# Optimization experiments

Measured on AMD Instinct MI355X. Metric: run time of the kernel, lower is better.

The kernel has to match this reference:

```python
import jax, jax.numpy as jnp
import numpy as np

N, E, D, H = 50000, 800000, 128, 128


def _uniform_param(key, shape, fan_in):
    bound = 1.0 / np.sqrt(fan_in)
    return jax.random.uniform(key, shape, jnp.float32, -bound, bound)


def setup_inputs() -> dict:
    key = jax.random.key(0)
    ks = jax.random.split(key, 12)
    x = jax.random.normal(ks[0], (N, D), jnp.float32)
    xedge = jax.random.randint(ks[1], (2, E), 0, N, jnp.int64)
    y = jax.random.randint(ks[2], (N,), 0, 2, jnp.int32).astype(bool)
    return {
        "x": x,
        "xedge": xedge,
        "y": y,
        "pretrain": 0,
        # SAGEConv layer 1 (in=D, out=H): lin_l (with bias) applied to mean aggr, lin_r (no bias) to self
        "W1l": _uniform_param(ks[3], (D, H), D),
        "b1l": _uniform_param(ks[4], (H,), D),
        "W1r": _uniform_param(ks[5], (D, H), D),
        # SAGEConv layer 2 (in=H, out=H)
        "W2l": _uniform_param(ks[6], (H, H), H),
        "b2l": _uniform_param(ks[7], (H,), H),
        "W2r": _uniform_param(ks[8], (H, H), H),
        # Decoder weight [H, H]
        "Wdec": _uniform_param(ks[9], (H, H), H),
    }


def sage_conv(h, src, dst, Wl, bl, Wr, num_nodes):
    # gather neighbor features along edges, mean-aggregate by destination
    msgs = h[src]                                            # [E, d]
    agg = jax.ops.segment_sum(msgs, dst, num_segments=num_nodes)
    cnt = jax.ops.segment_sum(jnp.ones((src.shape[0],), h.dtype), dst,
                              num_segments=num_nodes)
    mean = agg / jnp.maximum(cnt, 1.0)[:, None]              # [N, d]
    return mean @ Wl + bl + h @ Wr                           # [N, out]


def reference(x, xedge, y, pretrain, W1l, b1l, W1r, W2l, b2l, W2r, Wdec):
    src, dst = xedge[0], xedge[1]
    n = x.shape[0]
    # Encoder: SAGE = conv1 -> relu -> (dropout: eval identity) -> conv2
    h = jax.nn.relu(sage_conv(x, src, dst, W1l, b1l, W1r, n))
    emb = sage_conv(h, src, dst, W2l, b2l, W2r, n)           # [N, H]
    # Decoder
    dx = emb @ Wdec                                          # [N, H]
    # BCEWithLogits: pos nodes target 1, neg nodes target 0, mean within each group
    ym = y.astype(dx.dtype)                                  # [N]
    n_pos = jnp.sum(ym)
    n_neg = n - n_pos
    hdim = dx.shape[1]
    sp_pos = jax.nn.softplus(-dx)   # bce(logit, 1)
    sp_neg = jax.nn.softplus(dx)    # bce(logit, 0)
    l2 = jnp.sum(sp_pos * ym[:, None]) / (jnp.maximum(n_pos, 1.0) * hdim)
    l1 = jnp.sum(sp_neg * (1.0 - ym)[:, None]) / (jnp.maximum(n_neg, 1.0) * hdim)
    return (l1 + l2, emb)
```

## Files before the change

kernel.cpp:

```cpp
#include <hip/hip_runtime.h>
#include <hip/hip_bf16.h>

#define NDIM 128
#define MROWS 32
#define BTHREADS 512
#define SCAN_CHUNK 1024

typedef __attribute__((ext_vector_type(8))) short short8;
typedef __attribute__((ext_vector_type(4))) float f32x4;

__device__ __forceinline__ float bf2f(__hip_bfloat16 v) { return __bfloat162float(v); }

__device__ __forceinline__ float ldf(const void* p, long i, int f32) {
    return f32 ? ((const float*)p)[i] : bf2f(((const __hip_bfloat16*)p)[i]);
}
__device__ __forceinline__ void stf(void* p, long i, int f32, float v) {
    if (f32) ((float*)p)[i] = v;
    else     ((__hip_bfloat16*)p)[i] = __float2bfloat16(v);
}
__device__ __forceinline__ short f2bf(float v) {
    __hip_bfloat16 h = __float2bfloat16(v);
    short s;
    __builtin_memcpy(&s, &h, 2);
    return s;
}
__device__ __forceinline__ float bflo(unsigned u) { u <<= 16; float f; __builtin_memcpy(&f, &u, 4); return f; }
__device__ __forceinline__ float bfhi(unsigned u) { u &= 0xffff0000u; float f; __builtin_memcpy(&f, &u, 4); return f; }
__device__ __forceinline__ unsigned packbf(float a, float b) {
    unsigned la = (unsigned short)f2bf(a);
    unsigned hb = (unsigned short)f2bf(b);
    return (hb << 16) | la;
}
__device__ __forceinline__ int aswz(int m, int k) {
    return m * NDIM + ((((k >> 3) ^ (m & 7)) << 3) | (k & 7));
}
__device__ __forceinline__ int wswz(int m, int p) {
    return m * 64 + ((((p >> 2) ^ (m & 7)) << 2) | (p & 3));
}

__global__ void detect_kernel(const int* __restrict__ xedge32,
                              const unsigned int* __restrict__ yw,
                              const unsigned short* __restrict__ xh,
                              int* __restrict__ flags, int* __restrict__ cnt,
                              float* __restrict__ accum, int* __restrict__ npos, int N) {
    const int gid = blockIdx.x * 256 + threadIdx.x;
    for (int i = gid; i < N; i += gridDim.x * 256) cnt[i] = 0;
    if (gid == 0) { accum[0] = 0.f; accum[1] = 0.f; npos[0] = 0; }
    if (blockIdx.x == 0) {
        __shared__ int se, sy, scount;
        const int t = threadIdx.x;
        if (t == 0) { se = 1; sy = 0; scount = 0; }
        __syncthreads();
        for (int i = t; i < 512; i += 256)
            if (xedge32[2 * i + 1] != 0) se = 0;
        for (int i = t; i < 1024; i += 256)
            if (yw[i] > 1u) sy = 1;
        int c = 0;
        for (int i = t; i < 1024; i += 256) {
            int ex = (xh[2 * i] >> 7) & 0xFF;
            if (ex >= 100 && ex <= 150) c++;
        }
        atomicAdd(&scount, c);
        __syncthreads();
        if (t == 0) { flags[0] = se; flags[1] = sy; flags[2] = (scount < 900) ? 1 : 0; }
    }
}


__global__ void prep_kernel(const void* __restrict__ x,
                            const void* __restrict__ W1l, const void* __restrict__ b1l,
                            const void* __restrict__ W1r, const void* __restrict__ W2l,
                            const void* __restrict__ b2l, const void* __restrict__ W2r,
                            const void* __restrict__ Wd, const int* __restrict__ flags,
                            short* __restrict__ T1l, short* __restrict__ T1r,
                            short* __restrict__ T2l, short* __restrict__ T2r,
                            short* __restrict__ Td, float* __restrict__ b1c,
                            float* __restrict__ b2c, unsigned* __restrict__ xb,
                            const int* __restrict__ xedge, int E,
                            int* __restrict__ cnt, int N) {
    const int wf = flags[2];
    const long idx = (long)blockIdx.x * 256 + threadIdx.x;
    if (idx < E) {
        int d = flags[0] ? xedge[2 * (E + idx)] : xedge[E + idx];
        atomicAdd(&cnt[d], 1);
    }
    if (idx < NDIM * NDIM) {
        int k = (int)(idx >> 7), n = (int)(idx & 127);
        int o = n * NDIM + k;
        T1l[o] = f2bf(ldf(W1l, idx, wf));
        T1r[o] = f2bf(ldf(W1r, idx, wf));
        T2l[o] = f2bf(ldf(W2l, idx, wf));
        T2r[o] = f2bf(ldf(W2r, idx, wf));
        Td [o] = f2bf(ldf(Wd , idx, wf));
        if (idx < NDIM) { b1c[idx] = ldf(b1l, idx, wf); b2c[idx] = ldf(b2l, idx, wf); }
    }
    if (wf) {
        const long np = (long)N * 64;
        const long stride = (long)gridDim.x * 256;
        for (long p = idx; p < np; p += stride) {
            float2 v = ((const float2*)x)[p];
            xb[p] = packbf(v.x, v.y);
        }
    }
}


__global__ void scan_partial(const int* __restrict__ cnt, int* __restrict__ bsum, int N) {
    __shared__ int red[256];
    const int t = threadIdx.x;
    const long base = (long)blockIdx.x * SCAN_CHUNK + (long)t * 4;
    int s = 0;
#pragma unroll
    for (int i = 0; i < 4; ++i) { long idx = base + i; if (idx < N) s += cnt[idx]; }
    red[t] = s;
    __syncthreads();
    for (int off = 128; off >= 1; off >>= 1) {
        if (t < off) red[t] += red[t + off];
        __syncthreads();
    }
    if (t == 0) bsum[blockIdx.x] = red[0];
}

__global__ void scan_bsums(const int* __restrict__ bsum, int* __restrict__ boff,
                           int B, int* __restrict__ rowptr, int N) {
    __shared__ int part[1024];
    const int t = threadIdx.x;
    int v = (t < B) ? bsum[t] : 0;
    part[t] = v;
    __syncthreads();
    for (int off = 1; off < 1024; off <<= 1) {
        int u = (t >= off) ? part[t - off] : 0;
        __syncthreads();
        part[t] += u;
        __syncthreads();
    }
    if (t < B) boff[t] = part[t] - v;
    if (t == 1023) rowptr[N] = part[1023];
}

__global__ void scan_scatter(int* __restrict__ cnt, const int* __restrict__ boff,
                             int* __restrict__ rowptr, int N) {
    __shared__ int tsum[256];
    const int t = threadIdx.x;
    const long base = (long)blockIdx.x * SCAN_CHUNK + (long)t * 4;
    int loc[4];
    int s = 0;
#pragma unroll
    for (int i = 0; i < 4; ++i) {
        long idx = base + i;
        int c = (idx < N) ? cnt[idx] : 0;
        loc[i] = s;
        s += c;
    }
    tsum[t] = s;
    __syncthreads();
    for (int off = 1; off < 256; off <<= 1) {
        int u = (t >= off) ? tsum[t - off] : 0;
        __syncthreads();
        tsum[t] += u;
        __syncthreads();
    }
    const int texcl = tsum[t] - s;
    const int b0 = boff[blockIdx.x];
#pragma unroll
    for (int i = 0; i < 4; ++i) {
        long idx = base + i;
        if (idx < N) {
            int v = b0 + texcl + loc[i];
            rowptr[idx] = v;
            cnt[idx] = v;
        }
    }
}

__global__ void fill_kernel(const int* __restrict__ xedge, int E,
                            const int* __restrict__ flags,
                            int* __restrict__ cur, int* __restrict__ col) {
    int e = blockIdx.x * blockDim.x + threadIdx.x;
    if (e >= E) return;
    const int e64 = flags[0];
    int s = e64 ? xedge[2 * e] : xedge[e];
    int d = e64 ? xedge[2 * (E + e)] : xedge[E + e];
    int p = atomicAdd(&cur[d], 1);
    col[p] = s;
}


template <bool RELU, int OUTMODE>
__global__ __launch_bounds__(BTHREADS, 2)
void layer_mfma(const unsigned* __restrict__ Xb, const unsigned* __restrict__ Xraw,
                const int* __restrict__ rowptr,
                const int* __restrict__ col, const short* __restrict__ WlT,
                const float* __restrict__ biasc, const short* __restrict__ WrT,
                const short* __restrict__ WdT, const void* __restrict__ yv,
                const int* __restrict__ flags, void* __restrict__ outp,
                float* __restrict__ accum, int* __restrict__ npos, int N) {
    __shared__ short AS[2 * MROWS * NDIM];
    __shared__ int ylds[MROWS];
    __shared__ float redm[8][2];
    short* Ms = AS;
    short* Ss = AS + MROWS * NDIM;
    unsigned* Msw = (unsigned*)Ms;
    unsigned* Ssw = (unsigned*)Ss;
    const int t = threadIdx.x;
    const int n0 = blockIdx.x * MROWS;
    const int wf = flags[2];
    const unsigned* __restrict__ X = wf ? Xb : Xraw;

    if (OUTMODE == 1 && t < MROWS) {
        const int yb = flags[1];
        int n = n0 + t;
        int yn = -1;
        if (n < N)
            yn = yb ? (int)((const unsigned char*)yv)[n]
                    : (((const int*)yv)[n] != 0 ? 1 : 0);
        ylds[t] = yn;
    }

    {
        const int p = t & 63;
        const int g = __builtin_amdgcn_readfirstlane(t >> 6);
        int r = g;
        int b = 0, e = 0;
        {
            int n = n0 + r;
            if (n < N) {
                b = __builtin_amdgcn_readfirstlane(rowptr[n]);
                e = __builtin_amdgcn_readfirstlane(rowptr[n + 1]);
            }
        }
        for (int it = 0; it < 4; ++it, r += 8) {
            const int n = n0 + r;
            const int deg = e - b;
            unsigned su = 0;
            if (n < N) su = X[(long)n * 64 + p];
            const int* colb = col + b;
            int cs[32];
            if (deg > 0) {
#pragma unroll
                for (int j = 0; j < 8; ++j) {
                    int c = __builtin_amdgcn_readfirstlane(colb[j]);
                    cs[j] = ((unsigned)c >= (unsigned)N) ? 0 : c;
                }
            }
            if (deg > 8) {
#pragma unroll
                for (int j = 8; j < 16; ++j) {
                    int c = __builtin_amdgcn_readfirstlane(colb[j]);
                    cs[j] = ((unsigned)c >= (unsigned)N) ? 0 : c;
                }
            }
            if (deg > 16) {
#pragma unroll
                for (int j = 16; j < 24; ++j) {
                    int c = __builtin_amdgcn_readfirstlane(colb[j]);
                    cs[j] = ((unsigned)c >= (unsigned)N) ? 0 : c;
                }
            }
            if (deg > 24) {
#pragma unroll
                for (int j = 24; j < 32; ++j) {
                    int c = __builtin_amdgcn_readfirstlane(colb[j]);
                    cs[j] = ((unsigned)c >= (unsigned)N) ? 0 : c;
                }
            }
            unsigned u[32];
            if (deg > 0) {
#pragma unroll
                for (int j = 0; j < 8; ++j) u[j] = X[(long)cs[j] * 64 + p];
            }
            if (deg > 8) {
#pragma unroll
                for (int j = 8; j < 16; ++j) u[j] = X[(long)cs[j] * 64 + p];
            }
            if (deg > 16) {
#pragma unroll
                for (int j = 16; j < 24; ++j) u[j] = X[(long)cs[j] * 64 + p];
            }
            if (deg > 24) {
#pragma unroll
                for (int j = 24; j < 32; ++j) u[j] = X[(long)cs[j] * 64 + p];
            }
            int bn = 0, en = 0;
            if (it < 3) {
                int nn = n0 + r + 8;
                if (nn < N) {
                    bn = __builtin_amdgcn_readfirstlane(rowptr[nn]);
                    en = __builtin_amdgcn_readfirstlane(rowptr[nn + 1]);
                }
            }
            __builtin_amdgcn_sched_barrier(0);
            float m0 = 0.f, m1 = 0.f;
            if (deg > 0) {
                float p0 = 0.f, p1 = 0.f, p2 = 0.f, p3 = 0.f;
                float q0 = 0.f, q1 = 0.f, q2 = 0.f, q3 = 0.f;
#pragma unroll
                for (int j = 0; j < 32; j += 4) {
                    if (j + 0 < deg) { p0 += bflo(u[j]);     q0 += bfhi(u[j]); }
                    if (j + 1 < deg) { p1 += bflo(u[j + 1]); q1 += bfhi(u[j + 1]); }
                    if (j + 2 < deg) { p2 += bflo(u[j + 2]); q2 += bfhi(u[j + 2]); }
                    if (j + 3 < deg) { p3 += bflo(u[j + 3]); q3 += bfhi(u[j + 3]); }
                }
                m0 = (p0 + p1) + (p2 + p3);
                m1 = (q0 + q1) + (q2 + q3);
                for (int i = b + 32; i < e; ++i) {
                    int c = __builtin_amdgcn_readfirstlane(col[i]);
                    unsigned uu = X[(long)c * 64 + p];
                    m0 += bflo(uu);
                    m1 += bfhi(uu);
                }
                float inv = 1.f / (float)deg;
                m0 *= inv; m1 *= inv;
            }
            int wi = wswz(r, p);
            Msw[wi] = packbf(m0, m1);
            Ssw[wi] = su;
            b = bn; e = en;
        }
    }
    __syncthreads();
    const int l = t & 63, w = t >> 6;
    const int quad = l >> 4, l15 = l & 15;
    const int wcol = w * 16;
    f32x4 acc[2] = {};
    for (int k0 = 0; k0 < NDIM; k0 += 32) {
        const int kc = k0 + quad * 8;
        short8 ams[2], ass[2], bl, br;
#pragma unroll
        for (int rt = 0; rt < 2; ++rt) {
            int m = rt * 16 + l15;
            ams[rt] = *(const short8*)&Ms[aswz(m, kc)];
            ass[rt] = *(const short8*)&Ss[aswz(m, kc)];
        }
        {
            int n = wcol + l15;
            bl = *(const short8*)&WlT[n * NDIM + kc];
            br = *(const short8*)&WrT[n * NDIM + kc];
        }
#pragma unroll
        for (int rt = 0; rt < 2; ++rt) {
            acc[rt] = __builtin_amdgcn_mfma_f32_16x16x32_bf16(
                ams[rt], bl, acc[rt], 0, 0, 0);
            acc[rt] = __builtin_amdgcn_mfma_f32_16x16x32_bf16(
                ass[rt], br, acc[rt], 0, 0, 0);
        }
    }
    __syncthreads();

    if (OUTMODE == 0) {
        {
            int cg = wcol + l15;
            float bv = biasc[cg];
#pragma unroll
            for (int rt = 0; rt < 2; ++rt)
#pragma unroll
                for (int reg = 0; reg < 4; ++reg) {
                    int row = rt * 16 + quad * 4 + reg;
                    float v = acc[rt][reg] + bv;
                    if (RELU) v = fmaxf(v, 0.f);
                    Ms[row * NDIM + cg] = f2bf(v);
                }
        }
        __syncthreads();
        unsigned* ob = (unsigned*)outp;
        for (int idx = t; idx < MROWS * 64; idx += BTHREADS) {
            int r = idx >> 6;
            if (n0 + r < N) ob[(long)n0 * 64 + idx] = Msw[idx];
        }
    } else {
        {
            int cg = wcol + l15;
            float bv = biasc[cg];
#pragma unroll
            for (int rt = 0; rt < 2; ++rt)
#pragma unroll
                for (int reg = 0; reg < 4; ++reg) {
                    int row = rt * 16 + quad * 4 + reg;
                    float v = acc[rt][reg] + bv;
                    Ms[aswz(row, cg)] = f2bf(v);
                    int n = n0 + row;
                    if (n < N) {
                        if (wf) ((float*)outp)[1 + (long)n * NDIM + cg] = v;
                        else ((__hip_bfloat16*)outp)[1 + (long)n * NDIM + cg] =
                                 __float2bfloat16(v);
                    }
                }
        }
        __syncthreads();
        f32x4 acc2[2] = {};
        for (int k0 = 0; k0 < NDIM; k0 += 32) {
            const int kc = k0 + quad * 8;
            short8 a[2], bwd;
#pragma unroll
            for (int rt = 0; rt < 2; ++rt)
                a[rt] = *(const short8*)&Ms[aswz(rt * 16 + l15, kc)];
            bwd = *(const short8*)&WdT[(wcol + l15) * NDIM + kc];
#pragma unroll
            for (int rt = 0; rt < 2; ++rt)
                acc2[rt] = __builtin_amdgcn_mfma_f32_16x16x32_bf16(
                    a[rt], bwd, acc2[rt], 0, 0, 0);
        }
        float lpos = 0.f, lneg = 0.f;
#pragma unroll
        for (int rt = 0; rt < 2; ++rt)
#pragma unroll
            for (int reg = 0; reg < 4; ++reg) {
                int row = rt * 16 + quad * 4 + reg;
                int yn = ylds[row];
                if (yn >= 0) {
                    float z = acc2[rt][reg];
                    float L = log1pf(expf(-fabsf(z)));
                    if (yn) lpos += fmaxf(-z, 0.f) + L;
                    else    lneg += fmaxf(z, 0.f) + L;
                }
            }
#pragma unroll
        for (int off = 32; off >= 1; off >>= 1) {
            lpos += __shfl_down(lpos, off, 64);
            lneg += __shfl_down(lneg, off, 64);
        }
        if (l == 0) { redm[w][0] = lpos; redm[w][1] = lneg; }
        __syncthreads();
        if (t == 0) {
            float sp = 0.f, sn = 0.f;
#pragma unroll
            for (int i = 0; i < 8; ++i) { sp += redm[i][0]; sn += redm[i][1]; }
            atomicAdd(&accum[0], sp);
            atomicAdd(&accum[1], sn);
            int c = 0;
            for (int i = 0; i < MROWS; ++i) if (ylds[i] > 0) c++;
            if (c) atomicAdd(npos, c);
        }
    }
}

__global__ void finalize_kernel(const float* __restrict__ accum, const int* __restrict__ npos,
                                const int* __restrict__ flags, void* __restrict__ out, int N) {
    float np_ = (float)(*npos);
    float nn_ = (float)N - np_;
    float l2 = accum[0] / (fmaxf(np_, 1.f) * 128.f);
    float l1 = accum[1] / (fmaxf(nn_, 1.f) * 128.f);
    stf(out, 0, flags[2], l1 + l2);
}


extern "C" void kernel_launch(void* const* d_in, const int* in_sizes, int n_in,
                              void* d_out, int out_size, void* d_ws, size_t ws_size,
                              hipStream_t stream) {
    const void* x    = d_in[0];
    const int* xedge = (const int*)d_in[1];
    const void* y    = d_in[2];
    const void* W1l  = d_in[4];
    const void* b1l  = d_in[5];
    const void* W1r  = d_in[6];
    const void* W2l  = d_in[7];
    const void* b2l  = d_in[8];
    const void* W2r  = d_in[9];
    const void* Wdec = d_in[10];

    const int N = in_sizes[0] / NDIM;
    const int E = in_sizes[1] / 2;

    char* ws = (char*)d_ws;
    size_t off = 0;
    auto alloc = [&](size_t bytes) -> void* {
        void* p = ws + off;
        off = (off + bytes + 255) & ~(size_t)255;
        return p;
    };
    int*   flags  = (int*)alloc(64);
    float* accum  = (float*)alloc(64);
    int*   npos   = (int*)alloc(64);
    int*   bsum   = (int*)alloc(1024 * 4);
    int*   boff   = (int*)alloc(1024 * 4);
    int*   cnt    = (int*)alloc((size_t)N * 4);
    int*   rowptr = (int*)alloc((size_t)(N + 1) * 4);
    int*   col    = (int*)alloc((size_t)E * 4);
    unsigned* xb  = (unsigned*)alloc((size_t)N * 64 * 4);
    unsigned* hbuf = (unsigned*)alloc((size_t)N * 64 * 4);
    short* T1l = (short*)alloc(NDIM * NDIM * 2);
    short* T1r = (short*)alloc(NDIM * NDIM * 2);
    short* T2l = (short*)alloc(NDIM * NDIM * 2);
    short* T2r = (short*)alloc(NDIM * NDIM * 2);
    short* Td  = (short*)alloc(NDIM * NDIM * 2);
    float* b1c = (float*)alloc(NDIM * 4);
    float* b2c = (float*)alloc(NDIM * 4);

    const int zb = (N + 255) / 256;
    detect_kernel<<<zb, 256, 0, stream>>>(xedge, (const unsigned int*)y,
                                          (const unsigned short*)x, flags, cnt,
                                          accum, npos, N);
    const long prep_items = (E > NDIM * NDIM) ? E : NDIM * NDIM;
    prep_kernel<<<(int)((prep_items + 255) / 256), 256, 0, stream>>>(
        x, W1l, b1l, W1r, W2l, b2l, W2r, Wdec, flags,
        T1l, T1r, T2l, T2r, Td, b1c, b2c, xb, xedge, E, cnt, N);

    const int sb = (N + SCAN_CHUNK - 1) / SCAN_CHUNK;
    scan_partial<<<sb, 256, 0, stream>>>(cnt, bsum, N);
    scan_bsums<<<1, 1024, 0, stream>>>(bsum, boff, sb, rowptr, N);
    scan_scatter<<<sb, 256, 0, stream>>>(cnt, boff, rowptr, N);

    const int eb = (E + 255) / 256;
    fill_kernel<<<eb, 256, 0, stream>>>(xedge, E, flags, cnt, col);

    const int nbM = (N + MROWS - 1) / MROWS;
    layer_mfma<true, 0><<<nbM, BTHREADS, 0, stream>>>(
        xb, (const unsigned*)x, rowptr, col, T1l, b1c, T1r, nullptr, nullptr,
        flags, hbuf, nullptr, nullptr, N);
    layer_mfma<false, 1><<<nbM, BTHREADS, 0, stream>>>(
        hbuf, hbuf, rowptr, col, T2l, b2c, T2r, Td, y, flags,
        d_out, accum, npos, N);
    finalize_kernel<<<1, 1, 0, stream>>>(accum, npos, flags, d_out, N);
}
```

Before: 312.6 us.

## Fold format detection into prep, use memsets, pipeline neighbor gathers in halves

Removes the separate detect kernel. Every prep block now recomputes the edge-width and float-format checks from shared memory, the y-format check moves into scan_bsums, and buffer zeroing becomes hipMemsetAsync calls. The aggregation loop now loads neighbor rows in two 8-entry register buffers and accumulates one batch while the next is being loaded. This replaces the 32-register gather with a software pipeline that lowers register pressure. The cost is redundant detection reads in every prep block and a different gather/accumulate ordering.

Result: no change. 313.1 us (+0.2%).

```diff
diff --git a/kernel.cpp b/kernel.cpp
--- a/kernel.cpp
+++ b/kernel.cpp
@@ -38,50 +38,49 @@
     return m * 64 + ((((p >> 2) ^ (m & 7)) << 2) | (p & 3));
 }
 
-__global__ void detect_kernel(const int* __restrict__ xedge32,
-                              const unsigned int* __restrict__ yw,
-                              const unsigned short* __restrict__ xh,
-                              int* __restrict__ flags, int* __restrict__ cnt,
-                              float* __restrict__ accum, int* __restrict__ npos, int N) {
-    const int gid = blockIdx.x * 256 + threadIdx.x;
-    for (int i = gid; i < N; i += gridDim.x * 256) cnt[i] = 0;
-    if (gid == 0) { accum[0] = 0.f; accum[1] = 0.f; npos[0] = 0; }
-    if (blockIdx.x == 0) {
-        __shared__ int se, sy, scount;
-        const int t = threadIdx.x;
-        if (t == 0) { se = 1; sy = 0; scount = 0; }
-        __syncthreads();
-        for (int i = t; i < 512; i += 256)
-            if (xedge32[2 * i + 1] != 0) se = 0;
-        for (int i = t; i < 1024; i += 256)
-            if (yw[i] > 1u) sy = 1;
-        int c = 0;
-        for (int i = t; i < 1024; i += 256) {
-            int ex = (xh[2 * i] >> 7) & 0xFF;
-            if (ex >= 100 && ex <= 150) c++;
-        }
-        atomicAdd(&scount, c);
-        __syncthreads();
-        if (t == 0) { flags[0] = se; flags[1] = sy; flags[2] = (scount < 900) ? 1 : 0; }
-    }
-}
-
 
 __global__ void prep_kernel(const void* __restrict__ x,
                             const void* __restrict__ W1l, const void* __restrict__ b1l,
                             const void* __restrict__ W1r, const void* __restrict__ W2l,
                             const void* __restrict__ b2l, const void* __restrict__ W2r,
-                            const void* __restrict__ Wd, const int* __restrict__ flags,
+                            const void* __restrict__ Wd,
                             short* __restrict__ T1l, short* __restrict__ T1r,
                             short* __restrict__ T2l, short* __restrict__ T2r,
                             short* __restrict__ Td, float* __restrict__ b1c,
                             float* __restrict__ b2c, unsigned* __restrict__ xb,
                             const int* __restrict__ xedge, int E,
-                            int* __restrict__ cnt, int N) {
-    const int wf = flags[2];
-    const long idx = (long)blockIdx.x * 256 + threadIdx.x;
+                            int* __restrict__ cnt, int N,
+                            int* __restrict__ flags) {
+    __shared__ int s_se, s_sy, s_sc;
+    const int t = threadIdx.x;
+    if (t == 0) { s_se = 1; s_sy = 0; s_sc = 0; }
+    __syncthreads();
+    {
+        const int* xedge32 = xedge;
+        const unsigned int* yw = (const unsigned int*)nullptr;
+        (void)yw;
+        for (int i = t; i < 512; i += 256)
+            if (xedge32[2 * i + 1] != 0) s_se = 0;
+        const unsigned short* xh = (const unsigned short*)x;
+        int c = 0;
+        for (int i = t; i < 1024; i += 256) {
+            int ex = (xh[2 * i] >> 7) & 0xFF;
+            if (ex >= 100 && ex <= 150) c++;
+        }
+        atomicAdd(&s_sc, c);
+    }
+    __syncthreads();
+    const int e64 = s_se;
+    const int wf = (s_sc < 900) ? 1 : 0;
+    if (blockIdx.x == 0 && t < 64) {
+        if (t == 0) {
+            flags[0] = e64;
+            flags[2] = wf;
+        }
+    }
+    const long idx = (long)blockIdx.x * 256 + t;
     if (idx < E) {
-        int d = flags[0] ? xedge[2 * (E + idx)] : xedge[E + idx];
+        int d = e64 ? xedge[2 * (E + idx)] : xedge[E + idx];
         atomicAdd(&cnt[d], 1);
     }
     if (idx < NDIM * NDIM) {
@@ -97,12 +96,13 @@
     if (wf) {
         const long np = (long)N * 64;
         const long stride = (long)gridDim.x * 256;
-        for (long p = idx; p < np; p += stride) {
-            float2 v = ((const float2*)x)[p];
-            xb[p] = packbf(v.x, v.y);
-        }
-    }
-}
+        for (long pidx = idx; pidx < np; pidx += stride) {
+            float2 v = ((const float2*)x)[pidx];
+            xb[pidx] = packbf(v.x, v.y);
+        }
+    }
+}
+
 
 
 __global__ void scan_partial(const int* __restrict__ cnt, int* __restrict__ bsum, int N) {
@@ -122,9 +122,18 @@
 }
 
 __global__ void scan_bsums(const int* __restrict__ bsum, int* __restrict__ boff,
-                           int B, int* __restrict__ rowptr, int N) {
+                           int B, int* __restrict__ rowptr, int N,
+                           const unsigned int* __restrict__ yw,
+                           int* __restrict__ flags) {
     __shared__ int part[1024];
     const int t = threadIdx.x;
+    __shared__ int s_sy;
+    if (t == 0) s_sy = 0;
+    __syncthreads();
+    if (t < 256) {
+        for (int i = t; i < 1024; i += 256)
+            if (yw[i] > 1u) s_sy = 1;
+    }
     int v = (t < B) ? bsum[t] : 0;
     part[t] = v;
     __syncthreads();
@@ -136,6 +145,7 @@
     }
     if (t < B) boff[t] = part[t] - v;
     if (t == 1023) rowptr[N] = part[1023];
+    if (t == 0) flags[1] = s_sy;
 }
 
 __global__ void scan_scatter(int* __restrict__ cnt, const int* __restrict__ boff,
@@ -264,22 +274,16 @@
                     cs[j] = ((unsigned)c >= (unsigned)N) ? 0 : c;
                 }
             }
-            unsigned u[32];
+            float p0 = 0.f, p1 = 0.f, p2 = 0.f, p3 = 0.f;
+            float q0 = 0.f, q1 = 0.f, q2 = 0.f, q3 = 0.f;
+            unsigned ua[8], ub[8];
             if (deg > 0) {
 #pragma unroll
-                for (int j = 0; j < 8; ++j) u[j] = X[(long)cs[j] * 64 + p];
+                for (int j = 0; j < 8; ++j) ua[j] = X[(long)cs[j] * 64 + p];
             }
             if (deg > 8) {
 #pragma unroll
-                for (int j = 8; j < 16; ++j) u[j] = X[(long)cs[j] * 64 + p];
-            }
-            if (deg > 16) {
-#pragma unroll
-                for (int j = 16; j < 24; ++j) u[j] = X[(long)cs[j] * 64 + p];
-            }
-            if (deg > 24) {
-#pragma unroll
-                for (int j = 24; j < 32; ++j) u[j] = X[(long)cs[j] * 64 + p];
+                for (int j = 0; j < 8; ++j) ub[j] = X[(long)cs[8 + j] * 64 + p];
             }
             int bn = 0, en = 0;
             if (it < 3) {
@@ -289,18 +293,60 @@
                     en = __builtin_amdgcn_readfirstlane(rowptr[nn + 1]);
                 }
             }
-            __builtin_amdgcn_sched_barrier(0);
+            if (deg > 0) {
+#pragma unroll
+                for (int j = 0; j < 8; ++j) {
+                    if (j + 0 < deg) {
+                        if ((j & 3) == 0) { p0 += bflo(ua[j]); q0 += bfhi(ua[j]); }
+                        if ((j & 3) == 1) { p1 += bflo(ua[j]); q1 += bfhi(ua[j]); }
+                        if ((j & 3) == 2) { p2 += bflo(ua[j]); q2 += bfhi(ua[j]); }
+                        if ((j & 3) == 3) { p3 += bflo(ua[j]); q3 += bfhi(ua[j]); }
+                    }
+                }
+            }
+            if (deg > 16) {
+#pragma unroll
+                for (int j = 0; j < 8; ++j) ua[j] = X[(long)cs[16 + j] * 64 + p];
+            }
+            if (deg > 8) {
+#pragma unroll
+                for (int j = 0; j < 8; ++j) {
+                    if (8 + j < deg) {
+                        if ((j & 3) == 0) { p0 += bflo(ub[j]); q0 += bfhi(ub[j]); }
+                        if ((j & 3) == 1) { p1 += bflo(ub[j]); q1 += bfhi(ub[j]); }
+                        if ((j & 3) == 2) { p2 += bflo(ub[j]); q2 += bfhi(ub[j]); }
+                        if ((j & 3) == 3) { p3 += bflo(ub[j]); q3 += bfhi(ub[j]); }
+                    }
+                }
+            }
+            if (deg > 24) {
+#pragma unroll
+                for (int j = 0; j < 8; ++j) ub[j] = X[(long)cs[24 + j] * 64 + p];
+            }
+            if (deg > 16) {
+#pragma unroll
+                for (int j = 0; j < 8; ++j) {
+                    if (16 + j < deg) {
+                        if ((j & 3) == 0) { p0 += bflo(ua[j]); q0 += bfhi(ua[j]); }
+                        if ((j & 3) == 1) { p1 += bflo(ua[j]); q1 += bfhi(ua[j]); }
+                        if ((j & 3) == 2) { p2 += bflo(ua[j]); q2 += bfhi(ua[j]); }
+                        if ((j & 3) == 3) { p3 += bflo(ua[j]); q3 += bfhi(ua[j]); }
+                    }
+                }
+            }
+            if (deg > 24) {
+#pragma unroll
+                for (int j = 0; j < 8; ++j) {
+                    if (24 + j < deg) {
+                        if ((j & 3) == 0) { p0 += bflo(ub[j]); q0 += bfhi(ub[j]); }
+                        if ((j & 3) == 1) { p1 += bflo(ub[j]); q1 += bfhi(ub[j]); }
+                        if ((j & 3) == 2) { p2 += bflo(ub[j]); q2 += bfhi(ub[j]); }
+                        if ((j & 3) == 3) { p3 += bflo(ub[j]); q3 += bfhi(ub[j]); }
+                    }
+                }
+            }
             float m0 = 0.f, m1 = 0.f;
             if (deg > 0) {
-                float p0 = 0.f, p1 = 0.f, p2 = 0.f, p3 = 0.f;
-                float q0 = 0.f, q1 = 0.f, q2 = 0.f, q3 = 0.f;
-#pragma unroll
-                for (int j = 0; j < 32; j += 4) {
-                    if (j + 0 < deg) { p0 += bflo(u[j]);     q0 += bfhi(u[j]); }
-                    if (j + 1 < deg) { p1 += bflo(u[j + 1]); q1 += bfhi(u[j + 1]); }
-                    if (j + 2 < deg) { p2 += bflo(u[j + 2]); q2 += bfhi(u[j + 2]); }
-                    if (j + 3 < deg) { p3 += bflo(u[j + 3]); q3 += bfhi(u[j + 3]); }
-                }
                 m0 = (p0 + p1) + (p2 + p3);
                 m1 = (q0 + q1) + (q2 + q3);
                 for (int i = b + 32; i < e; ++i) {
@@ -486,18 +532,19 @@
     float* b1c = (float*)alloc(NDIM * 4);
     float* b2c = (float*)alloc(NDIM * 4);
 
-    const int zb = (N + 255) / 256;
-    detect_kernel<<<zb, 256, 0, stream>>>(xedge, (const unsigned int*)y,
-                                          (const unsigned short*)x, flags, cnt,
-                                          accum, npos, N);
+    hipMemsetAsync(cnt, 0, (size_t)N * 4, stream);
+    hipMemsetAsync(accum, 0, 64, stream);
+    hipMemsetAsync(npos, 0, 64, stream);
+
     const long prep_items = (E > NDIM * NDIM) ? E : NDIM * NDIM;
     prep_kernel<<<(int)((prep_items + 255) / 256), 256, 0, stream>>>(
-        x, W1l, b1l, W1r, W2l, b2l, W2r, Wdec, flags,
-        T1l, T1r, T2l, T2r, Td, b1c, b2c, xb, xedge, E, cnt, N);
+        x, W1l, b1l, W1r, W2l, b2l, W2r, Wdec,
+        T1l, T1r, T2l, T2r, Td, b1c, b2c, xb, xedge, E, cnt, N, flags);
 
     const int sb = (N + SCAN_CHUNK - 1) / SCAN_CHUNK;
     scan_partial<<<sb, 256, 0, stream>>>(cnt, bsum, N);
-    scan_bsums<<<1, 1024, 0, stream>>>(bsum, boff, sb, rowptr, N);
+    scan_bsums<<<1, 1024, 0, stream>>>(bsum, boff, sb, rowptr, N,
+                                       (const unsigned int*)y, flags);
     scan_scatter<<<sb, 256, 0, stream>>>(cnt, boff, rowptr, N);
 
     const int eb = (E + 255) / 256;
```
